# Kernel tuning notes

Measured on AMD Instinct MI355X. Metric: run time of the kernel, lower is better.

## Reference

```python
import jax, jax.numpy as jnp
import numpy as np
import math

B, T = 32768, 34
VOCAB = 14
SQRT_HD = math.sqrt(3.0)

def _pos_flat_index():
    # flatten (source, index) pairs into indices of a [14,3] table:
    # rows 0-9 = digit spiral enc, row 10 = z10_enc, rows 11-13 = special_enc
    flat = []
    for p in range(34):
        if p < 10:
            flat.append(p)
        elif p == 10:
            flat.append(11 + 0)
        elif p < 21:
            flat.append(p - 11)
        elif p == 21:
            flat.append(11 + 1)
        elif p < 33:
            z = p - 22
            flat.append(z if z < 10 else 10)
        else:
            flat.append(11 + 2)
    return np.array(flat, dtype=np.int32)

POS_FLAT = _pos_flat_index()

def setup_inputs() -> dict:
    key = jax.random.key(0)
    ks = jax.random.split(key, 12)
    r = lambda k, s: jax.random.normal(k, s, dtype=jnp.float32)
    return {
        'idx': jax.random.randint(ks[0], (B, T), 0, VOCAB, dtype=jnp.int64),
        'tok_emb': r(ks[1], (14, 3)),
        'pos_params': r(ks[2], (4,)),
        'z10_enc': r(ks[3], (1, 3)),
        'special_enc': r(ks[4], (3, 3)),
        'wq': r(ks[5], (3, 6)), 'wk': r(ks[6], (3, 6)), 'wv': r(ks[7], (3, 6)),
        'wo': r(ks[8], (6, 6)),
        'ln1_g': jnp.ones(6), 'ln1_b': jnp.zeros(6),
        'ln2_g': jnp.ones(6), 'ln2_b': jnp.zeros(6),
        'lnf_g': jnp.ones(6), 'lnf_b': jnp.zeros(6),
        'ffn_w1': r(ks[9], (6, 2)), 'ffn_b1': jnp.zeros(2),
        'ffn_w2': r(ks[10], (2, 6)), 'ffn_b2': jnp.zeros(6),
        'head_w': r(ks[11], (6, 3)),
    }

def _ln(x, g, b):
    mu = x.mean(-1, keepdims=True)
    var = ((x - mu) ** 2).mean(-1, keepdims=True)
    return (x - mu) * jax.lax.rsqrt(var + 1e-5) * g + b

def _forward(idx, tok_emb, pos_params, z10_enc, special_enc, wq, wk, wv, wo,
             ln1_g, ln1_b, ln2_g, ln2_b, lnf_g, lnf_b,
             ffn_w1, ffn_b1, ffn_w2, ffn_b2, head_w):
    amp, phase, slope, offset = pos_params[0], pos_params[1], pos_params[2], pos_params[3]
    i = jnp.arange(10, dtype=jnp.float32)
    ang = 2.0 * math.pi * i / 10.0 + phase
    digit = jnp.stack([amp * jnp.cos(ang), amp * jnp.sin(ang), slope * i + offset], -1)  # [10,3]
    table = jnp.concatenate([digit, z10_enc, special_enc], 0)  # [14,3]
    Tn = idx.shape[1]
    pos = table[POS_FLAT][:Tn]  # [T,3]
    tok = tok_emb[idx]  # [B,T,3]
    x = jnp.concatenate([tok, jnp.broadcast_to(pos, tok.shape)], -1)  # [B,T,6]
    h = _ln(x, ln1_g, ln1_b)
    h_tok, h_pos = h[..., :3], h[..., 3:]
    Bn = idx.shape[0]
    q = (h_pos @ wq).reshape(Bn, Tn, 2, 3)
    k = (h_pos @ wk).reshape(Bn, Tn, 2, 3)
    v = (h_tok @ wv).reshape(Bn, Tn, 2, 3)
    attn = jnp.einsum('bqhd,bkhd->bhqk', q, k) / SQRT_HD
    mask = jnp.tril(jnp.ones((Tn, Tn), bool))
    attn = jax.nn.softmax(jnp.where(mask, attn, -jnp.inf), axis=-1)
    o = jnp.einsum('bhqk,bkhd->bqhd', attn, v).reshape(Bn, Tn, 6)
    x = x + o @ wo
    h2 = _ln(x, ln2_g, ln2_b)
    x = x + (jax.nn.gelu(h2 @ ffn_w1 + ffn_b1, approximate=False) @ ffn_w2 + ffn_b2)
    x = _ln(x, lnf_g, lnf_b)
    return (x @ head_w) @ tok_emb.T  # [B,T,14]

def reference(idx, tok_emb, pos_params, z10_enc, special_enc, wq, wk, wv, wo,
              ln1_g, ln1_b, ln2_g, ln2_b, lnf_g, lnf_b,
              ffn_w1, ffn_b1, ffn_w2, ffn_b2, head_w):
    return _forward(idx, tok_emb, pos_params, z10_enc, special_enc, wq, wk, wv, wo,
                    ln1_g, ln1_b, ln2_g, ln2_b, lnf_g, lnf_b,
                    ffn_w1, ffn_b1, ffn_w2, ffn_b2, head_w)
```

## Files before the change

### kernel.cpp

```cpp
#include <hip/hip_runtime.h>
#include <math.h>

#define BT    34
#define TPR   17
#define RPB   15
#define BLOCK 256

typedef float v2f __attribute__((ext_vector_type(2)));
typedef float v4f __attribute__((ext_vector_type(4)));

#define QSCALE 0.83294037332470f

#if __has_builtin(__builtin_amdgcn_exp2f)
#define EXP2(x) __builtin_amdgcn_exp2f(x)
#else
#define EXP2(x) exp2f(x)
#endif

__device__ __forceinline__ void ln6(const float* x, const float* g, const float* b, float* o) {
  float mu = (x[0]+x[1]+x[2]+x[3]+x[4]+x[5]) * (1.0f/6.0f);
  float v = 0.f;
  #pragma unroll
  for (int c = 0; c < 6; ++c) { float d = x[c]-mu; v += d*d; }
  float inv = rsqrtf(v * (1.0f/6.0f) + 1e-5f);
  #pragma unroll
  for (int c = 0; c < 6; ++c) o[c] = (x[c]-mu)*inv*g[c] + b[c];
}

__global__ __launch_bounds__(BLOCK, 4)
void addtrans_kernel(const int* __restrict__ idx,
                     const float* __restrict__ tok_emb,
                     const float* __restrict__ pos_params,
                     const float* __restrict__ z10_enc,
                     const float* __restrict__ special_enc,
                     const float* __restrict__ wq,
                     const float* __restrict__ wk,
                     const float* __restrict__ wv,
                     const float* __restrict__ wo,
                     const float* __restrict__ ln1_g, const float* __restrict__ ln1_b,
                     const float* __restrict__ ln2_g, const float* __restrict__ ln2_b,
                     const float* __restrict__ lnf_g, const float* __restrict__ lnf_b,
                     const float* __restrict__ ffn_w1, const float* __restrict__ ffn_b1,
                     const float* __restrict__ ffn_w2, const float* __restrict__ ffn_b2,
                     const float* __restrict__ head_w,
                     float* __restrict__ out, int B)
{
  __shared__ __align__(16) float s_mem[RPB*BT*14];
  __shared__ float s_te[42];
  __shared__ float s_pos[BT*3];
  __shared__ float s_wq[18], s_wk[18], s_wv[18], s_wo[36], s_hw[18];
  __shared__ float s_g1[6], s_b1[6], s_g2[6], s_b2[6], s_gf[6], s_bf[6];
  __shared__ float s_w1[12], s_w2[12], s_fb1[2], s_fb2[6];

  const int tid = threadIdx.x;

  if (tid < 42) s_te[tid] = tok_emb[tid];
  if (tid < 18) { s_wq[tid]=wq[tid]; s_wk[tid]=wk[tid]; s_wv[tid]=wv[tid]; s_hw[tid]=head_w[tid]; }
  if (tid < 36) s_wo[tid] = wo[tid];
  if (tid < 12) { s_w1[tid]=ffn_w1[tid]; s_w2[tid]=ffn_w2[tid]; }
  if (tid < 6)  { s_g1[tid]=ln1_g[tid]; s_b1[tid]=ln1_b[tid];
                  s_g2[tid]=ln2_g[tid]; s_b2[tid]=ln2_b[tid];
                  s_gf[tid]=lnf_g[tid]; s_bf[tid]=lnf_b[tid];
                  s_fb2[tid]=ffn_b2[tid]; }
  if (tid < 2)  s_fb1[tid] = ffn_b1[tid];
  if (tid < BT) {
    int p = tid, f;
    if (p < 10) f = p;
    else if (p == 10) f = 11;
    else if (p < 21) f = p - 11;
    else if (p == 21) f = 12;
    else if (p < 33) { int z = p - 22; f = (z < 10) ? z : 10; }
    else f = 13;
    float e0, e1, e2;
    if (f < 10) {
      float amp = pos_params[0], ph = pos_params[1], sl = pos_params[2], of = pos_params[3];
      float ang = 0.62831853071795864769f * (float)f + ph;
      e0 = amp * cosf(ang); e1 = amp * sinf(ang); e2 = sl * (float)f + of;
    } else if (f == 10) { e0 = z10_enc[0]; e1 = z10_enc[1]; e2 = z10_enc[2]; }
    else { int u = f - 11; e0 = special_enc[u*3]; e1 = special_enc[u*3+1]; e2 = special_enc[u*3+2]; }
    s_pos[tid*3+0] = e0; s_pos[tid*3+1] = e1; s_pos[tid*3+2] = e2;
  }
  __syncthreads();

  const int row = tid / TPR;
  const int j   = tid - row * TPR;
  const int b   = blockIdx.x * RPB + row;
  const bool active = (row < RPB) && (b < B);

  v2f   qp[2][3];
  float xr[2][6];

  if (active) {
    const int base = b * BT;
    #pragma unroll
    for (int s = 0; s < 2; ++s) {
      const int t = j + s * TPR;
      const int vid = idx[base + t];
      float x6[6];
      x6[0] = s_te[vid*3+0]; x6[1] = s_te[vid*3+1]; x6[2] = s_te[vid*3+2];
      x6[3] = s_pos[t*3+0];  x6[4] = s_pos[t*3+1];  x6[5] = s_pos[t*3+2];
      float h[6];
      ln6(x6, s_g1, s_b1, h);
      float q6[6], k6[6], v6[6];
      #pragma unroll
      for (int c = 0; c < 6; ++c) {
        q6[c] = h[3]*s_wq[c] + h[4]*s_wq[6+c] + h[5]*s_wq[12+c];
        k6[c] = h[3]*s_wk[c] + h[4]*s_wk[6+c] + h[5]*s_wk[12+c];
        v6[c] = h[0]*s_wv[c] + h[1]*s_wv[6+c] + h[2]*s_wv[12+c];
        xr[s][c] = x6[c];
      }
      qp[s][0] = (v2f){q6[0]*QSCALE, q6[3]*QSCALE};
      qp[s][1] = (v2f){q6[1]*QSCALE, q6[4]*QSCALE};
      qp[s][2] = (v2f){q6[2]*QSCALE, q6[5]*QSCALE};
      v4f* kvp = (v4f*)&s_mem[(row*BT + t)*12];
      kvp[0] = (v4f){k6[0], k6[3], k6[1], k6[4]};
      kvp[1] = (v4f){k6[2], k6[5], v6[0], v6[3]};
      kvp[2] = (v4f){v6[1], v6[4], v6[2], v6[5]};
    }
  }
  __syncthreads();

  v2f l0 = (v2f){0.f,0.f}, l1 = (v2f){0.f,0.f};
  v2f o0[3] = {(v2f){0.f,0.f},(v2f){0.f,0.f},(v2f){0.f,0.f}};
  v2f o1[3] = {(v2f){0.f,0.f},(v2f){0.f,0.f},(v2f){0.f,0.f}};
  if (active) {
    const v4f* kvb = (const v4f*)&s_mem[row * (BT*12)];
    #pragma unroll 4
    for (int k = 0; k < TPR; ++k) {
      v4f A = kvb[k*3+0], Bv = kvb[k*3+1], C = kvb[k*3+2];
      v2f kA = (v2f){A.x, A.y}, kB = (v2f){A.z, A.w}, kC = (v2f){Bv.x, Bv.y};
      v2f vA = (v2f){Bv.z, Bv.w}, vB = (v2f){C.x, C.y}, vC = (v2f){C.z, C.w};
      v2f s0 = qp[0][0]*kA + qp[0][1]*kB + qp[0][2]*kC;
      const float mf = (k <= j) ? 1.f : 0.f;
      v2f p0 = (v2f){EXP2(s0.x), EXP2(s0.y)};
      p0 *= mf;
      l0 += p0; o0[0] += p0*vA; o0[1] += p0*vB; o0[2] += p0*vC;
      v2f s1 = qp[1][0]*kA + qp[1][1]*kB + qp[1][2]*kC;
      v2f p1 = (v2f){EXP2(s1.x), EXP2(s1.y)};
      l1 += p1; o1[0] += p1*vA; o1[1] += p1*vB; o1[2] += p1*vC;
    }
    #pragma unroll 4
    for (int k = TPR; k < BT; ++k) {
      v4f A = kvb[k*3+0], Bv = kvb[k*3+1], C = kvb[k*3+2];
      v2f kA = (v2f){A.x, A.y}, kB = (v2f){A.z, A.w}, kC = (v2f){Bv.x, Bv.y};
      v2f vA = (v2f){Bv.z, Bv.w}, vB = (v2f){C.x, C.y}, vC = (v2f){C.z, C.w};
      v2f s1 = qp[1][0]*kA + qp[1][1]*kB + qp[1][2]*kC;
      const float mf = (k <= j + TPR) ? 1.f : 0.f;
      v2f p1 = (v2f){EXP2(s1.x), EXP2(s1.y)};
      p1 *= mf;
      l1 += p1; o1[0] += p1*vA; o1[1] += p1*vB; o1[2] += p1*vC;
    }
  }
  __syncthreads();

  if (active) {
    #pragma unroll
    for (int s = 0; s < 2; ++s) {
      const int t = j + s * TPR;
      const v2f  lv = s ? l1 : l0;
      const v2f* ov = s ? o1 : o0;
      const float ia = __builtin_amdgcn_rcpf(lv.x);
      const float ib = __builtin_amdgcn_rcpf(lv.y);
      float a6[6] = { ov[0].x*ia, ov[1].x*ia, ov[2].x*ia,
                      ov[0].y*ib, ov[1].y*ib, ov[2].y*ib };
      float xn[6];
      #pragma unroll
      for (int c = 0; c < 6; ++c) {
        xn[c] = xr[s][c]
              + a6[0]*s_wo[c]    + a6[1]*s_wo[6+c]  + a6[2]*s_wo[12+c]
              + a6[3]*s_wo[18+c] + a6[4]*s_wo[24+c] + a6[5]*s_wo[30+c];
      }
      float h2[6];
      ln6(xn, s_g2, s_b2, h2);
      float a0 = s_fb1[0], a1 = s_fb1[1];
      #pragma unroll
      for (int d = 0; d < 6; ++d) { a0 += h2[d]*s_w1[d*2]; a1 += h2[d]*s_w1[d*2+1]; }
      const float g0 = 0.5f*a0*(1.0f + erff(a0*0.70710678118654752440f));
      const float g1 = 0.5f*a1*(1.0f + erff(a1*0.70710678118654752440f));
      #pragma unroll
      for (int c = 0; c < 6; ++c) xn[c] += g0*s_w2[c] + g1*s_w2[6+c] + s_fb2[c];
      float xf[6];
      ln6(xn, s_gf, s_bf, xf);
      float y0 = 0.f, y1 = 0.f, y2 = 0.f;
      #pragma unroll
      for (int c = 0; c < 6; ++c) {
        y0 += xf[c]*s_hw[c*3+0]; y1 += xf[c]*s_hw[c*3+1]; y2 += xf[c]*s_hw[c*3+2];
      }
      v2f* lp = (v2f*)&s_mem[(row*BT + t)*14];
      #pragma unroll
      for (int u = 0; u < 7; ++u) {
        const int c0 = 2*u, c1 = 2*u+1;
        lp[u] = (v2f){ y0*s_te[c0*3+0] + y1*s_te[c0*3+1] + y2*s_te[c0*3+2],
                       y0*s_te[c1*3+0] + y1*s_te[c1*3+1] + y2*s_te[c1*3+2] };
      }
    }
  }
  __syncthreads();

  {
    const int b0 = blockIdx.x * RPB;
    int nrows = B - b0; if (nrows > RPB) nrows = RPB;
    if (nrows > 0) {
      const int n4 = nrows * (BT*14/4);
      v4f* dst = reinterpret_cast<v4f*>(out + (size_t)b0 * (BT*14));
      const v4f* src = reinterpret_cast<const v4f*>(s_mem);
      for (int i = tid; i < n4; i += BLOCK)
        __builtin_nontemporal_store(src[i], dst + i);
    }
  }
}

extern "C" void kernel_launch(void* const* d_in, const int* in_sizes, int n_in,
                              void* d_out, int out_size, void* d_ws, size_t ws_size,
                              hipStream_t stream) {
  const int B = in_sizes[0] / BT;
  const int grid = (B + RPB - 1) / RPB;
  addtrans_kernel<<<grid, BLOCK, 0, stream>>>(
      (const int*)d_in[0],   (const float*)d_in[1], (const float*)d_in[2],
      (const float*)d_in[3], (const float*)d_in[4], (const float*)d_in[5],
      (const float*)d_in[6], (const float*)d_in[7], (const float*)d_in[8],
      (const float*)d_in[9], (const float*)d_in[10], (const float*)d_in[11],
      (const float*)d_in[12], (const float*)d_in[13], (const float*)d_in[14],
      (const float*)d_in[15], (const float*)d_in[16], (const float*)d_in[17],
      (const float*)d_in[18], (const float*)d_in[19],
      (float*)d_out, B);
}
```

Baseline: 141.0 us.

## Remap threads row-minor, stage idx in LDS, trim causal loops, pack math

Threads are now mapped with row = tid % RPB so that neighbouring lanes handle different batch rows. The K/V shared layout is made time-major to match, which changes the LDS bank access pattern. Token indices are staged into shared memory with a strided cooperative load. The causal attention loops now run only to the needed key instead of masking, with a software-prefetched K/V load. The LayerNorm, FFN and head math processes the two tokens each thread owns as packed v2f values, and launch bounds are raised to 5 waves. The trimmed loops make lane trip counts vary, which adds divergence within a wave, and the higher occupancy target may pressure registers.

```diff
diff --git a/kernel.cpp b/kernel.cpp
--- a/kernel.cpp
+++ b/kernel.cpp
@@ -17,17 +17,18 @@
 #define EXP2(x) exp2f(x)
 #endif
 
-__device__ __forceinline__ void ln6(const float* x, const float* g, const float* b, float* o) {
-  float mu = (x[0]+x[1]+x[2]+x[3]+x[4]+x[5]) * (1.0f/6.0f);
-  float v = 0.f;
+__device__ __forceinline__ void ln6p(const v2f* x, const float* g, const float* b, v2f* o) {
+  v2f mu = (x[0]+x[1]+x[2]+x[3]+x[4]+x[5]) * (1.0f/6.0f);
+  v2f v = (v2f){0.f, 0.f};
   #pragma unroll
-  for (int c = 0; c < 6; ++c) { float d = x[c]-mu; v += d*d; }
-  float inv = rsqrtf(v * (1.0f/6.0f) + 1e-5f);
+  for (int c = 0; c < 6; ++c) { v2f d = x[c]-mu; v += d*d; }
+  v2f inv = (v2f){ rsqrtf(v.x*(1.0f/6.0f) + 1e-5f),
+                   rsqrtf(v.y*(1.0f/6.0f) + 1e-5f) };
   #pragma unroll
   for (int c = 0; c < 6; ++c) o[c] = (x[c]-mu)*inv*g[c] + b[c];
 }
 
-__global__ __launch_bounds__(BLOCK, 4)
+__global__ __launch_bounds__(BLOCK, 5)
 void addtrans_kernel(const int* __restrict__ idx,
                      const float* __restrict__ tok_emb,
                      const float* __restrict__ pos_params,
@@ -46,6 +47,7 @@
                      float* __restrict__ out, int B)
 {
   __shared__ __align__(16) float s_mem[RPB*BT*14];
+  __shared__ int   s_idx[RPB*BT];
   __shared__ float s_te[42];
   __shared__ float s_pos[BT*3];
   __shared__ float s_wq[18], s_wk[18], s_wv[18], s_wo[36], s_hw[18];
@@ -53,6 +55,7 @@
   __shared__ float s_w1[12], s_w2[12], s_fb1[2], s_fb2[6];
 
   const int tid = threadIdx.x;
+  const int b0  = blockIdx.x * RPB;
 
   if (tid < 42) s_te[tid] = tok_emb[tid];
   if (tid < 18) { s_wq[tid]=wq[tid]; s_wk[tid]=wk[tid]; s_wv[tid]=wv[tid]; s_hw[tid]=head_w[tid]; }
@@ -63,6 +66,11 @@
                   s_gf[tid]=lnf_g[tid]; s_bf[tid]=lnf_b[tid];
                   s_fb2[tid]=ffn_b2[tid]; }
   if (tid < 2)  s_fb1[tid] = ffn_b1[tid];
+  {
+    int nr = B - b0; if (nr > RPB) nr = RPB;
+    const int tot = nr * BT;
+    for (int i = tid; i < tot; i += BLOCK) s_idx[i] = idx[b0*BT + i];
+  }
   if (tid < BT) {
     int p = tid, f;
     if (p < 10) f = p;
@@ -82,41 +90,45 @@
   }
   __syncthreads();
 
-  const int row = tid / TPR;
-  const int j   = tid - row * TPR;
-  const int b   = blockIdx.x * RPB + row;
-  const bool active = (row < RPB) && (b < B);
-
-  v2f   qp[2][3];
-  float xr[2][6];
+  const int row = tid % RPB;
+  const int j   = tid / RPB;
+  const int b   = b0 + row;
+  const bool active = (j < TPR) && (b < B);
+
+  v2f qpA[3], qpB[3];
+  v2f x6[6];
 
   if (active) {
-    const int base = b * BT;
-    #pragma unroll
-    for (int s = 0; s < 2; ++s) {
-      const int t = j + s * TPR;
-      const int vid = idx[base + t];
-      float x6[6];
-      x6[0] = s_te[vid*3+0]; x6[1] = s_te[vid*3+1]; x6[2] = s_te[vid*3+2];
-      x6[3] = s_pos[t*3+0];  x6[4] = s_pos[t*3+1];  x6[5] = s_pos[t*3+2];
-      float h[6];
-      ln6(x6, s_g1, s_b1, h);
-      float q6[6], k6[6], v6[6];
-      #pragma unroll
-      for (int c = 0; c < 6; ++c) {
-        q6[c] = h[3]*s_wq[c] + h[4]*s_wq[6+c] + h[5]*s_wq[12+c];
-        k6[c] = h[3]*s_wk[c] + h[4]*s_wk[6+c] + h[5]*s_wk[12+c];
-        v6[c] = h[0]*s_wv[c] + h[1]*s_wv[6+c] + h[2]*s_wv[12+c];
-        xr[s][c] = x6[c];
-      }
-      qp[s][0] = (v2f){q6[0]*QSCALE, q6[3]*QSCALE};
-      qp[s][1] = (v2f){q6[1]*QSCALE, q6[4]*QSCALE};
-      qp[s][2] = (v2f){q6[2]*QSCALE, q6[5]*QSCALE};
-      v4f* kvp = (v4f*)&s_mem[(row*BT + t)*12];
-      kvp[0] = (v4f){k6[0], k6[3], k6[1], k6[4]};
-      kvp[1] = (v4f){k6[2], k6[5], v6[0], v6[3]};
-      kvp[2] = (v4f){v6[1], v6[4], v6[2], v6[5]};
-    }
+    const int tA = j, tB = j + TPR;
+    const int vA = s_idx[row*BT + tA];
+    const int vB = s_idx[row*BT + tB];
+    #pragma unroll
+    for (int c = 0; c < 3; ++c) {
+      x6[c]   = (v2f){ s_te[vA*3+c],  s_te[vB*3+c]  };
+      x6[3+c] = (v2f){ s_pos[tA*3+c], s_pos[tB*3+c] };
+    }
+    v2f h[6];
+    ln6p(x6, s_g1, s_b1, h);
+    v2f q6[6], k6[6], v6[6];
+    #pragma unroll
+    for (int c = 0; c < 6; ++c) {
+      q6[c] = h[3]*s_wq[c] + h[4]*s_wq[6+c] + h[5]*s_wq[12+c];
+      k6[c] = h[3]*s_wk[c] + h[4]*s_wk[6+c] + h[5]*s_wk[12+c];
+      v6[c] = h[0]*s_wv[c] + h[1]*s_wv[6+c] + h[2]*s_wv[12+c];
+    }
+    #pragma unroll
+    for (int d = 0; d < 3; ++d) {
+      qpA[d] = (v2f){ q6[d].x, q6[3+d].x } * QSCALE;
+      qpB[d] = (v2f){ q6[d].y, q6[3+d].y } * QSCALE;
+    }
+    v4f* pA = (v4f*)&s_mem[(tA*RPB + row)*12];
+    pA[0] = (v4f){ k6[0].x, k6[3].x, k6[1].x, k6[4].x };
+    pA[1] = (v4f){ k6[2].x, k6[5].x, v6[0].x, v6[3].x };
+    pA[2] = (v4f){ v6[1].x, v6[4].x, v6[2].x, v6[5].x };
+    v4f* pB = (v4f*)&s_mem[(tB*RPB + row)*12];
+    pB[0] = (v4f){ k6[0].y, k6[3].y, k6[1].y, k6[4].y };
+    pB[1] = (v4f){ k6[2].y, k6[5].y, v6[0].y, v6[3].y };
+    pB[2] = (v4f){ v6[1].y, v6[4].y, v6[2].y, v6[5].y };
   }
   __syncthreads();
 
@@ -124,81 +136,90 @@
   v2f o0[3] = {(v2f){0.f,0.f},(v2f){0.f,0.f},(v2f){0.f,0.f}};
   v2f o1[3] = {(v2f){0.f,0.f},(v2f){0.f,0.f},(v2f){0.f,0.f}};
   if (active) {
-    const v4f* kvb = (const v4f*)&s_mem[row * (BT*12)];
-    #pragma unroll 4
-    for (int k = 0; k < TPR; ++k) {
-      v4f A = kvb[k*3+0], Bv = kvb[k*3+1], C = kvb[k*3+2];
-      v2f kA = (v2f){A.x, A.y}, kB = (v2f){A.z, A.w}, kC = (v2f){Bv.x, Bv.y};
-      v2f vA = (v2f){Bv.z, Bv.w}, vB = (v2f){C.x, C.y}, vC = (v2f){C.z, C.w};
-      v2f s0 = qp[0][0]*kA + qp[0][1]*kB + qp[0][2]*kC;
-      const float mf = (k <= j) ? 1.f : 0.f;
+    const float* kvbase = s_mem + row*12;
+    v4f A  = ((const v4f*)kvbase)[0];
+    v4f Bv = ((const v4f*)kvbase)[1];
+    v4f C  = ((const v4f*)kvbase)[2];
+    for (int k = 0; k <= j; ++k) {
+      const v4f Ac = A, Bc = Bv, Cc = C;
+      const v4f* nxt = (const v4f*)(kvbase + (k+1)*(RPB*12));
+      A = nxt[0]; Bv = nxt[1]; C = nxt[2];
+      v2f kA = (v2f){Ac.x, Ac.y}, kB = (v2f){Ac.z, Ac.w}, kC = (v2f){Bc.x, Bc.y};
+      v2f vA = (v2f){Bc.z, Bc.w}, vB = (v2f){Cc.x, Cc.y}, vC = (v2f){Cc.z, Cc.w};
+      v2f s0 = qpA[0]*kA + qpA[1]*kB + qpA[2]*kC;
       v2f p0 = (v2f){EXP2(s0.x), EXP2(s0.y)};
-      p0 *= mf;
       l0 += p0; o0[0] += p0*vA; o0[1] += p0*vB; o0[2] += p0*vC;
-      v2f s1 = qp[1][0]*kA + qp[1][1]*kB + qp[1][2]*kC;
+      v2f s1 = qpB[0]*kA + qpB[1]*kB + qpB[2]*kC;
       v2f p1 = (v2f){EXP2(s1.x), EXP2(s1.y)};
       l1 += p1; o1[0] += p1*vA; o1[1] += p1*vB; o1[2] += p1*vC;
     }
-    #pragma unroll 4
-    for (int k = TPR; k < BT; ++k) {
-      v4f A = kvb[k*3+0], Bv = kvb[k*3+1], C = kvb[k*3+2];
-      v2f kA = (v2f){A.x, A.y}, kB = (v2f){A.z, A.w}, kC = (v2f){Bv.x, Bv.y};
-      v2f vA = (v2f){Bv.z, Bv.w}, vB = (v2f){C.x, C.y}, vC = (v2f){C.z, C.w};
-      v2f s1 = qp[1][0]*kA + qp[1][1]*kB + qp[1][2]*kC;
-      const float mf = (k <= j + TPR) ? 1.f : 0.f;
+    for (int i = 1; i <= TPR; ++i) {
+      const int k = j + i;
+      const v4f Ac = A, Bc = Bv, Cc = C;
+      const v4f* nxt = (const v4f*)(kvbase + (k+1)*(RPB*12));
+      A = nxt[0]; Bv = nxt[1]; C = nxt[2];
+      v2f kA = (v2f){Ac.x, Ac.y}, kB = (v2f){Ac.z, Ac.w}, kC = (v2f){Bc.x, Bc.y};
+      v2f vA = (v2f){Bc.z, Bc.w}, vB = (v2f){Cc.x, Cc.y}, vC = (v2f){Cc.z, Cc.w};
+      v2f s1 = qpB[0]*kA + qpB[1]*kB + qpB[2]*kC;
       v2f p1 = (v2f){EXP2(s1.x), EXP2(s1.y)};
-      p1 *= mf;
       l1 += p1; o1[0] += p1*vA; o1[1] += p1*vB; o1[2] += p1*vC;
     }
   }
   __syncthreads();
 
   if (active) {
-    #pragma unroll
-    for (int s = 0; s < 2; ++s) {
-      const int t = j + s * TPR;
-      const v2f  lv = s ? l1 : l0;
-      const v2f* ov = s ? o1 : o0;
-      const float ia = __builtin_amdgcn_rcpf(lv.x);
-      const float ib = __builtin_amdgcn_rcpf(lv.y);
-      float a6[6] = { ov[0].x*ia, ov[1].x*ia, ov[2].x*ia,
-                      ov[0].y*ib, ov[1].y*ib, ov[2].y*ib };
-      float xn[6];
-      #pragma unroll
-      for (int c = 0; c < 6; ++c) {
-        xn[c] = xr[s][c]
-              + a6[0]*s_wo[c]    + a6[1]*s_wo[6+c]  + a6[2]*s_wo[12+c]
-              + a6[3]*s_wo[18+c] + a6[4]*s_wo[24+c] + a6[5]*s_wo[30+c];
-      }
-      float h2[6];
-      ln6(xn, s_g2, s_b2, h2);
-      float a0 = s_fb1[0], a1 = s_fb1[1];
-      #pragma unroll
-      for (int d = 0; d < 6; ++d) { a0 += h2[d]*s_w1[d*2]; a1 += h2[d]*s_w1[d*2+1]; }
-      const float g0 = 0.5f*a0*(1.0f + erff(a0*0.70710678118654752440f));
-      const float g1 = 0.5f*a1*(1.0f + erff(a1*0.70710678118654752440f));
-      #pragma unroll
-      for (int c = 0; c < 6; ++c) xn[c] += g0*s_w2[c] + g1*s_w2[6+c] + s_fb2[c];
-      float xf[6];
-      ln6(xn, s_gf, s_bf, xf);
-      float y0 = 0.f, y1 = 0.f, y2 = 0.f;
-      #pragma unroll
-      for (int c = 0; c < 6; ++c) {
-        y0 += xf[c]*s_hw[c*3+0]; y1 += xf[c]*s_hw[c*3+1]; y2 += xf[c]*s_hw[c*3+2];
-      }
-      v2f* lp = (v2f*)&s_mem[(row*BT + t)*14];
-      #pragma unroll
-      for (int u = 0; u < 7; ++u) {
-        const int c0 = 2*u, c1 = 2*u+1;
-        lp[u] = (v2f){ y0*s_te[c0*3+0] + y1*s_te[c0*3+1] + y2*s_te[c0*3+2],
-                       y0*s_te[c1*3+0] + y1*s_te[c1*3+1] + y2*s_te[c1*3+2] };
-      }
+    const float rA0 = __builtin_amdgcn_rcpf(l0.x);
+    const float rA1 = __builtin_amdgcn_rcpf(l0.y);
+    const float rB0 = __builtin_amdgcn_rcpf(l1.x);
+    const float rB1 = __builtin_amdgcn_rcpf(l1.y);
+    v2f a6[6];
+    a6[0] = (v2f){ o0[0].x*rA0, o1[0].x*rB0 };
+    a6[1] = (v2f){ o0[1].x*rA0, o1[1].x*rB0 };
+    a6[2] = (v2f){ o0[2].x*rA0, o1[2].x*rB0 };
+    a6[3] = (v2f){ o0[0].y*rA1, o1[0].y*rB1 };
+    a6[4] = (v2f){ o0[1].y*rA1, o1[1].y*rB1 };
+    a6[5] = (v2f){ o0[2].y*rA1, o1[2].y*rB1 };
+    v2f xn[6];
+    #pragma unroll
+    for (int c = 0; c < 6; ++c) {
+      xn[c] = x6[c]
+            + a6[0]*s_wo[c]    + a6[1]*s_wo[6+c]  + a6[2]*s_wo[12+c]
+            + a6[3]*s_wo[18+c] + a6[4]*s_wo[24+c] + a6[5]*s_wo[30+c];
+    }
+    v2f h2[6];
+    ln6p(xn, s_g2, s_b2, h2);
+    v2f a0 = (v2f){s_fb1[0], s_fb1[0]};
+    v2f a1 = (v2f){s_fb1[1], s_fb1[1]};
+    #pragma unroll
+    for (int d = 0; d < 6; ++d) { a0 += h2[d]*s_w1[d*2]; a1 += h2[d]*s_w1[d*2+1]; }
+    const float KIS2 = 0.70710678118654752440f;
+    v2f g0 = (v2f){ 0.5f*a0.x*(1.0f + erff(a0.x*KIS2)),
+                    0.5f*a0.y*(1.0f + erff(a0.y*KIS2)) };
+    v2f g1 = (v2f){ 0.5f*a1.x*(1.0f + erff(a1.x*KIS2)),
+                    0.5f*a1.y*(1.0f + erff(a1.y*KIS2)) };
+    #pragma unroll
+    for (int c = 0; c < 6; ++c) xn[c] += g0*s_w2[c] + g1*s_w2[6+c] + s_fb2[c];
+    v2f xf[6];
+    ln6p(xn, s_gf, s_bf, xf);
+    v2f y0 = (v2f){0.f,0.f}, y1 = (v2f){0.f,0.f}, y2 = (v2f){0.f,0.f};
+    #pragma unroll
+    for (int c = 0; c < 6; ++c) {
+      y0 += xf[c]*s_hw[c*3+0]; y1 += xf[c]*s_hw[c*3+1]; y2 += xf[c]*s_hw[c*3+2];
+    }
+    v2f* lpA = (v2f*)&s_mem[(row*BT + j      )*14];
+    v2f* lpB = (v2f*)&s_mem[(row*BT + j + TPR)*14];
+    #pragma unroll
+    for (int u = 0; u < 7; ++u) {
+      const int c0 = 2*u, c1 = 2*u+1;
+      v2f lg0 = y0*s_te[c0*3+0] + y1*s_te[c0*3+1] + y2*s_te[c0*3+2];
+      v2f lg1 = y0*s_te[c1*3+0] + y1*s_te[c1*3+1] + y2*s_te[c1*3+2];
+      lpA[u] = (v2f){ lg0.x, lg1.x };
+      lpB[u] = (v2f){ lg0.y, lg1.y };
     }
   }
   __syncthreads();
 
   {
-    const int b0 = blockIdx.x * RPB;
     int nrows = B - b0; if (nrows > RPB) nrows = RPB;
     if (nrows > 0) {
       const int n4 = nrows * (BT*14/4);
```

After: 133.6 us. 5.3% less time.
